# Optimization experiments

Measured on AMD Instinct MI355X. Metric: run time of the kernel, lower is better.

Reference implementation:

```python
import jax, jax.numpy as jnp
import numpy as np

VOCAB = 30522
HIDDEN = 768
MAX_POS = 512
N_TYPES = 8
N_HEADS = 4
NHID = 128
LN_EPS = 1e-12
ALPHA = 0.01  # LeakyReLU slope
NEG = -9e15


def setup_inputs() -> dict:
    key = jax.random.key(0)
    ks = jax.random.split(key, 12)
    B, N = 8, 256
    token_ids = jax.random.randint(ks[0], (B, N), 0, VOCAB)
    type_ids = jax.random.randint(ks[1], (B, N), 0, 7)
    synset_ids = jax.random.randint(ks[2], (B, N), 0, 32)
    highway = jax.random.randint(ks[3], (B, N), 0, 2).astype(bool)
    tok_emb = jax.random.normal(ks[4], (VOCAB, HIDDEN), jnp.float32) * 0.02
    type_emb = jax.random.normal(ks[5], (N_TYPES, HIDDEN), jnp.float32) * 0.02
    pos_emb = jax.random.normal(ks[6], (MAX_POS, HIDDEN), jnp.float32) * 0.02
    ln_g = jnp.ones((HIDDEN,), jnp.float32)
    ln_b = jnp.zeros((HIDDEN,), jnp.float32)
    # GAT per-head params, xavier-ish scale
    W = jax.random.normal(ks[7], (N_HEADS, HIDDEN, NHID), jnp.float32) * (1.414 * (2.0 / (HIDDEN + NHID)) ** 0.5)
    a = jax.random.normal(ks[8], (N_HEADS, 2 * NHID), jnp.float32) * (1.414 * (2.0 / (2 * NHID + 1)) ** 0.5)
    out_W = jax.random.normal(ks[9], (VOCAB, N_HEADS * NHID), jnp.float32) * 0.02
    out_b = jnp.zeros((VOCAB,), jnp.float32)
    return {"token_ids": token_ids, "type_ids": type_ids, "synset_ids": synset_ids,
            "highway": highway, "tok_emb": tok_emb, "type_emb": type_emb,
            "pos_emb": pos_emb, "ln_g": ln_g, "ln_b": ln_b, "W": W, "a": a,
            "out_W": out_W, "out_b": out_b}


def _graph_mask(token_ids, type_ids, synset_ids, highway):
    # visibility: same synset, plus directed highway edges by type
    vis = synset_ids[:, :, None] == synset_ids[:, None, :]
    t, hw = type_ids, highway
    s1 = (t == 1) & hw
    s3 = (t == 3) & hw
    d1 = (jnp.isin(t, jnp.array([0, 2, 5]))) & hw
    d3 = (jnp.isin(t, jnp.array([6, 4, 0]))) & hw
    vis = vis | (s1[:, :, None] & d1[:, None, :]) | (s3[:, :, None] & d3[:, None, :])
    not_pad = token_ids != 0  # bert padding_idx == 0
    return vis & not_pad[:, None, :]  # (B,N,N)


def reference(token_ids, type_ids, synset_ids, highway, tok_emb, type_emb,
              pos_emb, ln_g, ln_b, W, a, out_W, out_b):
    B, N = token_ids.shape
    mask = _graph_mask(token_ids, type_ids, synset_ids, highway)
    # TaxoEmbedding (eval mode: no dropout)
    x = tok_emb[token_ids] + type_emb[type_ids] + pos_emb[:N][None]
    mu = jnp.mean(x, axis=-1, keepdims=True)
    var = jnp.mean((x - mu) ** 2, axis=-1, keepdims=True)
    x = (x - mu) * jax.lax.rsqrt(var + LN_EPS) * ln_g + ln_b
    # GAT heads. e[h,b,i,j] = leakyrelu(a1_h . Wh[b,i] + a2_h . Wh[b,j])
    Wh = jnp.einsum('bnd,hdf->hbnf', x, W)  # (H,B,N,F)
    F_ = W.shape[-1]
    a1, a2 = a[:, :F_], a[:, F_:]
    e = (jnp.einsum('hbnf,hf->hbn', Wh, a1)[:, :, :, None]
         + jnp.einsum('hbnf,hf->hbn', Wh, a2)[:, :, None, :])
    e = jnp.where(e > 0, e, ALPHA * e)
    e = jnp.where(mask[None], e, NEG)
    att = jax.nn.softmax(e, axis=2)  # torch softmax(dim=1) on (B,N,N) -> i axis
    hp = jax.nn.elu(jnp.einsum('hbij,hbjf->hbif', att, Wh))  # (H,B,N,F)
    cat = hp.transpose(1, 2, 0, 3).reshape(B, N, -1)  # head-major concat
    out = jax.nn.elu(cat @ out_W.T + out_b)
    return jax.nn.log_softmax(out, axis=-1)
```

## Files before the change

### kernel.cpp

```cpp
#include <hip/hip_runtime.h>
#include <hip/hip_bf16.h>

#define VOCAB 30522
#define VPAD 30720
#define HIDDEN 768
#define NHEADS 4
#define NHID 128
#define ROWS 2048
#define KDIM 512
#define LN_EPS 1e-12f
#define ALPHA_LR 0.01f
#define NEGV -9.0e15f
#define NT256 120

typedef __attribute__((ext_vector_type(8))) short short8;
typedef __attribute__((ext_vector_type(4))) float floatx4;
typedef __attribute__((ext_vector_type(2))) float floatx2;
typedef __attribute__((ext_vector_type(4))) unsigned short ushort4v;
typedef __attribute__((ext_vector_type(8))) unsigned short ushort8v;
typedef __attribute__((ext_vector_type(4))) unsigned int uint4v;

static __device__ __forceinline__ unsigned short f2bf(float f) {
  unsigned int u = __float_as_uint(f);
  unsigned int r = u + 0x7fffu + ((u >> 16) & 1u);
  return (unsigned short)(r >> 16);
}

static __device__ __forceinline__ void gload16(const unsigned short* g, unsigned short* l) {
  __builtin_amdgcn_global_load_lds(
      (const __attribute__((address_space(1))) void*)g,
      (__attribute__((address_space(3))) void*)l, 16, 0, 0);
}

__global__ __launch_bounds__(256) void k_prep(const float* __restrict__ out_W,
    unsigned short* __restrict__ owb,
    const float* __restrict__ W, unsigned short* __restrict__ Wt,
    const int* __restrict__ tok, const int* __restrict__ typ,
    const float* __restrict__ tok_emb, const float* __restrict__ type_emb, const float* __restrict__ pos_emb,
    const float* __restrict__ ln_g, const float* __restrict__ ln_b, unsigned short* __restrict__ xout) {
  __shared__ unsigned short T[128][136];
  __shared__ float red[8];
  int bid = blockIdx.x;
  if (bid < 2048) {
    int n4src = (VOCAB * KDIM) / 4, n4tot = (VPAD * KDIM) / 4;
    int i = bid * 256 + threadIdx.x;
    int stride = 2048 * 256;
    for (; i < n4tot; i += stride) {
      ushort4v o = {0, 0, 0, 0};
      if (i < n4src) {
        floatx4 v = reinterpret_cast<const floatx4*>(out_W)[i];
        o.x = f2bf(v.x); o.y = f2bf(v.y); o.z = f2bf(v.z); o.w = f2bf(v.w);
      }
      reinterpret_cast<ushort4v*>(owb)[i] = o;
    }
  } else if (bid < 2072) {
    int b = bid - 2048;
    int h = b & 3, dc = b >> 2;
    int tid = threadIdx.x;
    const float* Wb = W + ((long)h * HIDDEN + dc * 128) * NHID;
    #pragma unroll
    for (int q = 0; q < 16; q++) {
      int idx = q * 256 + tid;
      int d = idx >> 5, f4 = idx & 31;
      floatx4 v = *reinterpret_cast<const floatx4*>(&Wb[(long)d * NHID + f4 * 4]);
      #pragma unroll
      for (int j = 0; j < 4; j++) T[f4 * 4 + j][d] = f2bf(v[j]);
    }
    __syncthreads();
    int f = tid >> 1, rh = tid & 1;
    unsigned short* dst = Wt + (long)(h * 128 + f) * HIDDEN + dc * 128 + rh * 64;
    #pragma unroll
    for (int i = 0; i < 8; i++)
      *reinterpret_cast<ushort8v*>(&dst[i * 8]) =
          *reinterpret_cast<const ushort8v*>(&T[f][rh * 64 + i * 8]);
  } else {
    int row = bid - 2072;
    int n = row & 255;
    int t = tok[row], ty = typ[row];
    const float* te = tok_emb + (long)t * HIDDEN;
    const float* ye = type_emb + (long)ty * HIDDEN;
    const float* pe = pos_emb + (long)n * HIDDEN;
    float v[3]; float s = 0.f, ss = 0.f;
    #pragma unroll
    for (int q = 0; q < 3; q++) {
      int d = threadIdx.x + q * 256;
      float x = te[d] + ye[d] + pe[d];
      v[q] = x; s += x; ss += x * x;
    }
    for (int off = 32; off; off >>= 1) { s += __shfl_down(s, off); ss += __shfl_down(ss, off); }
    int wid = threadIdx.x >> 6;
    if ((threadIdx.x & 63) == 0) { red[wid] = s; red[4 + wid] = ss; }
    __syncthreads();
    if (threadIdx.x == 0) {
      float a = red[0] + red[1] + red[2] + red[3];
      float b2 = red[4] + red[5] + red[6] + red[7];
      float mu = a * (1.0f / 768.0f);
      float var = b2 * (1.0f / 768.0f) - mu * mu;
      red[0] = mu; red[1] = rsqrtf(var + LN_EPS);
    }
    __syncthreads();
    float mu = red[0], rstd = red[1];
    #pragma unroll
    for (int q = 0; q < 3; q++) {
      int d = threadIdx.x + q * 256;
      xout[(long)row * HIDDEN + d] = f2bf((v[q] - mu) * rstd * ln_g[d] + ln_b[d]);
    }
  }
}

__global__ __launch_bounds__(256) void k_wh(const unsigned short* __restrict__ A,
    const unsigned short* __restrict__ Bw, float* __restrict__ Wh) {
  int mt = blockIdx.x & 15, nt = blockIdx.x >> 4;
  int m0 = mt * 128, n0 = nt * 128;
  __shared__ __align__(16) unsigned short Al[2][128 * 64];
  __shared__ __align__(16) unsigned short Bl[2][128 * 64];
  int tid = threadIdx.x;
  int l = tid & 63, wid = tid >> 6;
  int wr = wid >> 1, wc = wid & 1;
  int lrow = l & 15, lgrp = l >> 4;
  floatx4 acc[4][4];
  #pragma unroll
  for (int i = 0; i < 4; i++)
    #pragma unroll
    for (int j = 0; j < 4; j++) acc[i][j] = (floatx4){0.f, 0.f, 0.f, 0.f};
  const unsigned short* Ab = A + (long)m0 * HIDDEN;
  const unsigned short* Bb = Bw + (long)n0 * HIDDEN;

  auto STAGE = [&](int t, int bufi) {
    #pragma unroll
    for (int q = 0; q < 4; q++) {
      int chunk = q * 256 + tid;
      int row = chunk >> 3, kp = chunk & 7, swz = kp ^ (row & 7);
      long off = (long)row * HIDDEN + t * 64 + swz * 8;
      gload16(Ab + off, &Al[bufi][chunk * 8]);
      gload16(Bb + off, &Bl[bufi][chunk * 8]);
    }
  };

  STAGE(0, 0);
  STAGE(1, 1);
  asm volatile("s_waitcnt vmcnt(8)" ::: "memory");
  __builtin_amdgcn_sched_barrier(0);
  __builtin_amdgcn_s_barrier();

  #pragma unroll
  for (int kt = 0; kt < 12; kt++) {
    int cur = kt & 1;
    short8 af[2][4], bf[2][4];
    #pragma unroll
    for (int kk = 0; kk < 2; kk++) {
      int sA = (kk * 4 + lgrp) ^ (lrow & 7);
      #pragma unroll
      for (int mi = 0; mi < 4; mi++)
        af[kk][mi] = *reinterpret_cast<const short8*>(&Al[cur][(wr * 64 + mi * 16 + lrow) * 64 + sA * 8]);
      #pragma unroll
      for (int ni = 0; ni < 4; ni++)
        bf[kk][ni] = *reinterpret_cast<const short8*>(&Bl[cur][(wc * 64 + ni * 16 + lrow) * 64 + sA * 8]);
    }
    asm volatile("s_waitcnt lgkmcnt(0)" ::: "memory");
    __builtin_amdgcn_sched_barrier(0);
    __builtin_amdgcn_s_barrier();
    __builtin_amdgcn_sched_barrier(0);
    if (kt < 10) STAGE(kt + 2, cur);
    #pragma unroll
    for (int kk = 0; kk < 2; kk++)
      #pragma unroll
      for (int mi = 0; mi < 4; mi++)
        #pragma unroll
        for (int ni = 0; ni < 4; ni++)
          acc[mi][ni] = __builtin_amdgcn_mfma_f32_16x16x32_bf16(af[kk][mi], bf[kk][ni], acc[mi][ni], 0, 0, 0);
    if (kt < 10) {
      asm volatile("s_waitcnt vmcnt(8)" ::: "memory");
    } else if (kt == 10) {
      asm volatile("s_waitcnt vmcnt(0)" ::: "memory");
    }
    __builtin_amdgcn_sched_barrier(0);
    if (kt < 11) __builtin_amdgcn_s_barrier();
  }

  #pragma unroll
  for (int mi = 0; mi < 4; mi++) {
    #pragma unroll
    for (int reg = 0; reg < 4; reg++) {
      int row = m0 + wr * 64 + mi * 16 + lgrp * 4 + reg;
      #pragma unroll
      for (int ni = 0; ni < 4; ni++) {
        int c = n0 + wc * 64 + ni * 16 + lrow;
        int h = c >> 7, f = c & 127;
        Wh[((long)h * ROWS + row) * NHID + f] = acc[mi][ni][reg];
      }
    }
  }
}

__device__ __forceinline__ unsigned char mk_flags(int t, int hwv, int tokv) {
  unsigned char fl = 0;
  if (hwv) {
    if (t == 1) fl |= 1;
    if (t == 3) fl |= 2;
    if (t == 0 || t == 2 || t == 5) fl |= 4;
    if (t == 6 || t == 4 || t == 0) fl |= 8;
  }
  if (tokv != 0) fl |= 16;
  return fl;
}

__global__ __launch_bounds__(256) void k_ecol(const int* __restrict__ tok, const int* __restrict__ typ,
    const int* __restrict__ syn, const int* __restrict__ hw,
    const float* __restrict__ Wh, const float* __restrict__ a,
    float* __restrict__ e1, float* __restrict__ e2,
    float* __restrict__ colmax, float* __restrict__ colrs) {
  int h = blockIdx.x >> 3, b = blockIdx.x & 7;
  __shared__ float av[256];
  __shared__ float E1[256]; __shared__ int SY[256]; __shared__ unsigned char FL[256];
  int tid = threadIdx.x;
  int g = b * 256 + tid;
  av[tid] = a[h * 256 + tid];
  FL[tid] = mk_flags(typ[g], hw[g], tok[g]);
  SY[tid] = syn[g];
  __syncthreads();
  const float* wr = Wh + ((long)h * ROWS + g) * NHID;
  float s1 = 0.f, s2 = 0.f;
  #pragma unroll 8
  for (int f = 0; f < 128; f++) { float w = wr[f]; s1 += w * av[f]; s2 += w * av[128 + f]; }
  e1[h * ROWS + g] = s1; e2[h * ROWS + g] = s2;
  E1[tid] = s1;
  __syncthreads();
  float e2j = s2;
  int syj = SY[tid]; unsigned char flj = FL[tid];
  bool npj = flj & 16, d1j = flj & 4, d3j = flj & 8;
  float m = -INFINITY;
  for (int i = 0; i < 256; i++) {
    float e = E1[i] + e2j;
    e = e > 0.f ? e : ALPHA_LR * e;
    unsigned char fli = FL[i];
    bool vis = (SY[i] == syj) || ((fli & 1) && d1j) || ((fli & 2) && d3j);
    float v = (vis && npj) ? e : NEGV;
    m = fmaxf(m, v);
  }
  float s = 0.f;
  for (int i = 0; i < 256; i++) {
    float e = E1[i] + e2j;
    e = e > 0.f ? e : ALPHA_LR * e;
    unsigned char fli = FL[i];
    bool vis = (SY[i] == syj) || ((fli & 1) && d1j) || ((fli & 2) && d3j);
    float v = (vis && npj) ? e : NEGV;
    s += __expf(v - m);
  }
  int idx = (h * 8 + b) * 256 + tid;
  colmax[idx] = m;
  colrs[idx] = 1.0f / s;
}

__global__ __launch_bounds__(256) void k_att(const int* __restrict__ tok, const int* __restrict__ typ,
    const int* __restrict__ syn, const int* __restrict__ hw,
    const float* __restrict__ e1, const float* __restrict__ e2,
    const float* __restrict__ colmax, const float* __restrict__ colrs,
    const float* __restrict__ Wh, unsigned short* __restrict__ cat) {
  int chunk = blockIdx.x & 7; int hb = blockIdx.x >> 3;
  int h = hb >> 3, b = hb & 7;
  __shared__ float E2[256], CM[256], CR[256];
  __shared__ int SY[256]; __shared__ unsigned char FL[256];
  __shared__ float WJ[64][128];
  int tid = threadIdx.x;
  {
    int g = b * 256 + tid;
    FL[tid] = mk_flags(typ[g], hw[g], tok[g]);
    E2[tid] = e2[h * ROWS + g];
    CM[tid] = colmax[hb * 256 + tid];
    CR[tid] = colrs[hb * 256 + tid];
    SY[tid] = syn[g];
  }
  __syncthreads();
  int i = chunk * 32 + (tid >> 3);
  int gi = b * 256 + i;
  float e1i = e1[h * ROWS + gi];
  unsigned char fli = FL[i];
  bool s1i = fli & 1, s3i = fli & 2;
  int syni = SY[i];
  int f0 = tid & 7;
  floatx4 acc4[4];
  #pragma unroll
  for (int k2 = 0; k2 < 4; k2++) acc4[k2] = (floatx4){0.f, 0.f, 0.f, 0.f};
  for (int j0 = 0; j0 < 256; j0 += 64) {
    #pragma unroll
    for (int q = 0; q < 8; q++) {
      int e = tid + q * 256;
      int j = e >> 5, f4 = e & 31;
      *reinterpret_cast<floatx4*>(&WJ[j][f4 * 4]) =
          *reinterpret_cast<const floatx4*>(&Wh[((long)h * ROWS + b * 256 + j0 + j) * NHID + f4 * 4]);
    }
    __syncthreads();
    for (int j = 0; j < 64; j++) {
      int jj = j0 + j;
      unsigned char flj = FL[jj];
      bool vis = (syni == SY[jj]) || (s1i && (flj & 4)) || (s3i && (flj & 8));
      bool msk = vis && (flj & 16);
      float ev = e1i + E2[jj];
      ev = ev > 0.f ? ev : ALPHA_LR * ev;
      float v = msk ? ev : NEGV;
      float w = __expf(v - CM[jj]) * CR[jj];
      #pragma unroll
      for (int k2 = 0; k2 < 4; k2++) {
        floatx4 wv = *reinterpret_cast<const floatx4*>(&WJ[j][(f0 + 8 * k2) * 4]);
        acc4[k2] += wv * w;
      }
    }
    __syncthreads();
  }
  ushort4v* cr4 = reinterpret_cast<ushort4v*>(cat + (long)gi * KDIM + h * NHID);
  #pragma unroll
  for (int k2 = 0; k2 < 4; k2++) {
    ushort4v o4;
    #pragma unroll
    for (int e = 0; e < 4; e++) {
      float v = acc4[k2][e];
      v = v > 0.f ? v : __expf(v) - 1.f;
      o4[e] = f2bf(v);
    }
    cr4[f0 + 8 * k2] = o4;
  }
}

__global__ __launch_bounds__(512, 2) void k_gemm(const unsigned short* __restrict__ A,
    const unsigned short* __restrict__ Bw, const float* __restrict__ bias,
    unsigned short* __restrict__ otmp, float* __restrict__ ps) {
  int bid = blockIdx.x;
  int lin = (bid & 7) * NT256 + (bid >> 3);
  int mt = lin & 7, nt = lin >> 3;
  int m0 = mt * 256, n0 = nt * 256;
  __shared__ __align__(16) char smem[131072];
  unsigned short (*Al)[256 * 64] = reinterpret_cast<unsigned short (*)[256 * 64]>(smem);
  unsigned short (*Bl)[256 * 64] = reinterpret_cast<unsigned short (*)[256 * 64]>(smem + 65536);
  unsigned short* Cl = reinterpret_cast<unsigned short*>(smem);
  int tid = threadIdx.x;
  int l = tid & 63, wid = tid >> 6;
  int wr = wid >> 2, wc = wid & 3;
  int lrow = l & 15, lgrp = l >> 4;
  floatx4 acc[8][4];
  #pragma unroll
  for (int i = 0; i < 8; i++)
    #pragma unroll
    for (int j = 0; j < 4; j++) acc[i][j] = (floatx4){0.f, 0.f, 0.f, 0.f};
  const unsigned short* Ab = A + (long)m0 * KDIM;
  const unsigned short* Bb = Bw + (long)n0 * KDIM;

  auto STAGE = [&](int t, int bufi) {
    #pragma unroll
    for (int q = 0; q < 4; q++) {
      int chunk = q * 512 + tid;
      int row = chunk >> 3, kp = chunk & 7, swz = kp ^ (row & 7);
      long off = (long)row * KDIM + t * 64 + swz * 8;
      gload16(Ab + off, &Al[bufi][chunk * 8]);
      gload16(Bb + off, &Bl[bufi][chunk * 8]);
    }
  };

  STAGE(0, 0);
  STAGE(1, 1);
  asm volatile("s_waitcnt vmcnt(8)" ::: "memory");
  __builtin_amdgcn_sched_barrier(0);
  __builtin_amdgcn_s_barrier();

  #pragma unroll
  for (int kt = 0; kt < 8; kt++) {
    int cur = kt & 1;
    short8 afr[8];
    short8 bfr[4];
    #pragma unroll
    for (int mi = 0; mi < 4; mi++)
      #pragma unroll
      for (int ks = 0; ks < 2; ks++)
        afr[mi * 2 + ks] = *reinterpret_cast<const short8*>(
            &Al[cur][(wr * 128 + mi * 16 + lrow) * 64 + (((ks * 4 + lgrp) ^ (lrow & 7)) * 8)]);
    #pragma unroll
    for (int ni = 0; ni < 2; ni++)
      #pragma unroll
      for (int ks = 0; ks < 2; ks++)
        bfr[ni * 2 + ks] = *reinterpret_cast<const short8*>(
            &Bl[cur][(wc * 64 + ni * 16 + lrow) * 64 + (((ks * 4 + lgrp) ^ (lrow & 7)) * 8)]);
    #pragma unroll
    for (int ks = 0; ks < 2; ks++)
      #pragma unroll
      for (int mi = 0; mi < 4; mi++)
        #pragma unroll
        for (int ni = 0; ni < 2; ni++)
          acc[mi][ni] = __builtin_amdgcn_mfma_f32_16x16x32_bf16(afr[mi * 2 + ks], bfr[ni * 2 + ks], acc[mi][ni], 0, 0, 0);
    __builtin_amdgcn_sched_barrier(0);
    #pragma unroll
    for (int ni = 0; ni < 2; ni++)
      #pragma unroll
      for (int ks = 0; ks < 2; ks++)
        bfr[ni * 2 + ks] = *reinterpret_cast<const short8*>(
            &Bl[cur][(wc * 64 + (2 + ni) * 16 + lrow) * 64 + (((ks * 4 + lgrp) ^ (lrow & 7)) * 8)]);
    #pragma unroll
    for (int ks = 0; ks < 2; ks++)
      #pragma unroll
      for (int mi = 0; mi < 4; mi++)
        #pragma unroll
        for (int ni = 0; ni < 2; ni++)
          acc[mi][2 + ni] = __builtin_amdgcn_mfma_f32_16x16x32_bf16(afr[mi * 2 + ks], bfr[ni * 2 + ks], acc[mi][2 + ni], 0, 0, 0);
    __builtin_amdgcn_sched_barrier(0);
    #pragma unroll
    for (int mi = 0; mi < 4; mi++)
      #pragma unroll
      for (int ks = 0; ks < 2; ks++)
        afr[mi * 2 + ks] = *reinterpret_cast<const short8*>(
            &Al[cur][(wr * 128 + (4 + mi) * 16 + lrow) * 64 + (((ks * 4 + lgrp) ^ (lrow & 7)) * 8)]);
    #pragma unroll
    for (int ks = 0; ks < 2; ks++)
      #pragma unroll
      for (int mi = 0; mi < 4; mi++)
        #pragma unroll
        for (int ni = 0; ni < 2; ni++)
          acc[4 + mi][2 + ni] = __builtin_amdgcn_mfma_f32_16x16x32_bf16(afr[mi * 2 + ks], bfr[ni * 2 + ks], acc[4 + mi][2 + ni], 0, 0, 0);
    __builtin_amdgcn_sched_barrier(0);
    #pragma unroll
    for (int ni = 0; ni < 2; ni++)
      #pragma unroll
      for (int ks = 0; ks < 2; ks++)
        bfr[ni * 2 + ks] = *reinterpret_cast<const short8*>(
            &Bl[cur][(wc * 64 + ni * 16 + lrow) * 64 + (((ks * 4 + lgrp) ^ (lrow & 7)) * 8)]);
    asm volatile("s_waitcnt lgkmcnt(0)" ::: "memory");
    __builtin_amdgcn_sched_barrier(0);
    __builtin_amdgcn_s_barrier();
    __builtin_amdgcn_sched_barrier(0);
    if (kt < 6) STAGE(kt + 2, cur);
    #pragma unroll
    for (int ks = 0; ks < 2; ks++)
      #pragma unroll
      for (int mi = 0; mi < 4; mi++)
        #pragma unroll
        for (int ni = 0; ni < 2; ni++)
          acc[4 + mi][ni] = __builtin_amdgcn_mfma_f32_16x16x32_bf16(afr[mi * 2 + ks], bfr[ni * 2 + ks], acc[4 + mi][ni], 0, 0, 0);
    if (kt < 6) {
      asm volatile("s_waitcnt vmcnt(8)" ::: "memory");
    } else if (kt == 6) {
      asm volatile("s_waitcnt vmcnt(0)" ::: "memory");
    }
    __builtin_amdgcn_sched_barrier(0);
    if (kt < 7) __builtin_amdgcn_s_barrier();
  }
  float bcol[4];
  #pragma unroll
  for (int ni = 0; ni < 4; ni++) {
    int c = n0 + wc * 64 + ni * 16 + lrow;
    bcol[ni] = (c < VOCAB) ? bias[c] : 0.f;
  }
  #pragma unroll
  for (int mi = 0; mi < 8; mi++)
    #pragma unroll
    for (int ni = 0; ni < 4; ni++)
      #pragma unroll
      for (int reg = 0; reg < 4; reg++) {
        int r = wr * 128 + mi * 16 + lgrp * 4 + reg;
        int c = wc * 64 + ni * 16 + lrow;
        float z = acc[mi][ni][reg] + bcol[ni];
        float o = z > 0.f ? z : __expf(z) - 1.f;
        Cl[r * 256 + c] = f2bf(o);
      }
  __syncthreads();
  #pragma unroll
  for (int it = 0; it < 16; it++) {
    int idx = it * 512 + tid;
    int r = idx >> 5, c8 = (idx & 31) * 8;
    int gc = n0 + c8;
    ushort8v v = *reinterpret_cast<const ushort8v*>(&Cl[r * 256 + c8]);
    float se = 0.f;
    #pragma unroll
    for (int e = 0; e < 8; e++)
      if (gc + e < VOCAB)
        se += __expf(__uint_as_float(((unsigned int)(unsigned short)v[e]) << 16));
    #pragma unroll
    for (int off = 1; off < 32; off <<= 1) se += __shfl_xor(se, off);
    if ((idx & 31) == 0) ps[(long)(m0 + r) * 128 + nt] = se;
    unsigned short* orow = otmp + (long)(m0 + r) * 2 * VOCAB;
    if (gc + 8 <= VOCAB) {
      *reinterpret_cast<ushort8v*>(orow + gc) = v;
    } else {
      #pragma unroll
      for (int e = 0; e < 8; e++)
        if (gc + e < VOCAB) orow[gc + e] = v[e];
    }
  }
}

__global__ __launch_bounds__(128) void k_lse(const float* __restrict__ ps, float* __restrict__ lse) {
  int row = blockIdx.x;
  int tid = threadIdx.x;
  float s = (tid < NT256) ? ps[(long)row * 128 + tid] : 0.f;
  #pragma unroll
  for (int off = 1; off < 64; off <<= 1) s += __shfl_xor(s, off);
  __shared__ float red[2];
  if ((tid & 63) == 0) red[tid >> 6] = s;
  __syncthreads();
  if (tid == 0) lse[row] = logf(red[0] + red[1]);
}

__global__ __launch_bounds__(1024) void k_sub(float* __restrict__ out, const float* __restrict__ lse) {
  int row = blockIdx.x;
  float L = lse[row];
  float* rb = out + (long)row * VOCAB;
  const uint4v* src4 = reinterpret_cast<const uint4v*>(rb);
  int tid = threadIdx.x;
  uint4v v4[4];
  #pragma unroll
  for (int k = 0; k < 4; k++) {
    int p4 = tid + k * 1024;
    if (p4 < 3816) v4[k] = src4[p4];
  }
  __syncthreads();
  floatx4* dst4 = reinterpret_cast<floatx4*>(rb);
  #pragma unroll
  for (int k = 0; k < 4; k++) {
    int p4 = tid + k * 1024;
    if (p4 < 3815) {
      uint4v u = v4[k];
      floatx4 a, b;
      a.x = __uint_as_float((u.x & 0xffffu) << 16) - L;
      a.y = __uint_as_float(u.x & 0xffff0000u) - L;
      a.z = __uint_as_float((u.y & 0xffffu) << 16) - L;
      a.w = __uint_as_float(u.y & 0xffff0000u) - L;
      b.x = __uint_as_float((u.z & 0xffffu) << 16) - L;
      b.y = __uint_as_float(u.z & 0xffff0000u) - L;
      b.z = __uint_as_float((u.w & 0xffffu) << 16) - L;
      b.w = __uint_as_float(u.w & 0xffff0000u) - L;
      dst4[2 * p4] = a;
      dst4[2 * p4 + 1] = b;
    } else if (p4 == 3815) {
      unsigned int u = v4[k].x;
      rb[30520] = __uint_as_float((u & 0xffffu) << 16) - L;
      rb[30521] = __uint_as_float(u & 0xffff0000u) - L;
    }
  }
}

extern "C" void kernel_launch(void* const* d_in, const int* in_sizes, int n_in,
                              void* d_out, int out_size, void* d_ws, size_t ws_size,
                              hipStream_t stream) {
  const int* tok = (const int*)d_in[0];
  const int* typ = (const int*)d_in[1];
  const int* syn = (const int*)d_in[2];
  const int* hw  = (const int*)d_in[3];
  const float* tok_emb  = (const float*)d_in[4];
  const float* type_emb = (const float*)d_in[5];
  const float* pos_emb  = (const float*)d_in[6];
  const float* ln_g = (const float*)d_in[7];
  const float* ln_b = (const float*)d_in[8];
  const float* W    = (const float*)d_in[9];
  const float* a    = (const float*)d_in[10];
  const float* out_W = (const float*)d_in[11];
  const float* out_b = (const float*)d_in[12];
  float* out = (float*)d_out;
  char* ws = (char*)d_ws;
  unsigned short* xb = (unsigned short*)(ws + 0);
  float* Wh  = (float*)(ws + 3145728);
  float* e1  = (float*)(ws + 7340032);
  float* e2  = (float*)(ws + 7372800);
  float* cm  = (float*)(ws + 7405568);
  float* cs  = (float*)(ws + 7438336);
  unsigned short* cat = (unsigned short*)(ws + 7471104);
  unsigned short* Wt  = (unsigned short*)(ws + 9568256);
  unsigned short* owb = (unsigned short*)(ws + 10354688);
  float* ps  = (float*)(ws + 41811968);
  float* lse = (float*)(ws + 42860544);

  k_prep<<<4120, 256, 0, stream>>>(out_W, owb, W, Wt, tok, typ,
                                   tok_emb, type_emb, pos_emb, ln_g, ln_b, xb);
  k_wh<<<64, 256, 0, stream>>>(xb, Wt, Wh);
  k_ecol<<<32, 256, 0, stream>>>(tok, typ, syn, hw, Wh, a, e1, e2, cm, cs);
  k_att<<<256, 256, 0, stream>>>(tok, typ, syn, hw, e1, e2, cm, cs, Wh, cat);
  k_gemm<<<8 * NT256, 512, 0, stream>>>(cat, owb, out_b, (unsigned short*)out, ps);
  k_lse<<<2048, 128, 0, stream>>>(ps, lse);
  k_sub<<<2048, 1024, 0, stream>>>(out, lse);
}
```

Measured before the change: 313.5 us.

## Move row exp-sum from GEMM epilogue into fused log-softmax kernel

The per-tile partial exp-sum computation and its cross-lane shuffles are removed from the GEMM epilogue, and the separate k_lse kernel is dropped. k_sub now computes the row's exp-sum itself from the bf16 values already loaded into registers, reduces it across the block, takes the log, then subtracts. This removes one kernel launch, the partial-sum buffer and work in the GEMM epilogue. In exchange k_sub does more exp arithmetic and an extra block-wide reduction with a barrier.

After: 304.4 us. 2.9% less time.

```diff
diff --git a/kernel.cpp b/kernel.cpp
--- a/kernel.cpp
+++ b/kernel.cpp
@@ -324,7 +324,7 @@
 
 __global__ __launch_bounds__(512, 2) void k_gemm(const unsigned short* __restrict__ A,
     const unsigned short* __restrict__ Bw, const float* __restrict__ bias,
-    unsigned short* __restrict__ otmp, float* __restrict__ ps) {
+    unsigned short* __restrict__ otmp) {
   int bid = blockIdx.x;
   int lin = (bid & 7) * NT256 + (bid >> 3);
   int mt = lin & 7, nt = lin >> 3;
@@ -466,14 +466,6 @@
     int r = idx >> 5, c8 = (idx & 31) * 8;
     int gc = n0 + c8;
     ushort8v v = *reinterpret_cast<const ushort8v*>(&Cl[r * 256 + c8]);
-    float se = 0.f;
-    #pragma unroll
-    for (int e = 0; e < 8; e++)
-      if (gc + e < VOCAB)
-        se += __expf(__uint_as_float(((unsigned int)(unsigned short)v[e]) << 16));
-    #pragma unroll
-    for (int off = 1; off < 32; off <<= 1) se += __shfl_xor(se, off);
-    if ((idx & 31) == 0) ps[(long)(m0 + r) * 128 + nt] = se;
     unsigned short* orow = otmp + (long)(m0 + r) * 2 * VOCAB;
     if (gc + 8 <= VOCAB) {
       *reinterpret_cast<ushort8v*>(orow + gc) = v;
@@ -485,31 +477,49 @@
   }
 }
 
-__global__ __launch_bounds__(128) void k_lse(const float* __restrict__ ps, float* __restrict__ lse) {
+__global__ __launch_bounds__(1024) void k_sub(float* __restrict__ out) {
   int row = blockIdx.x;
-  int tid = threadIdx.x;
-  float s = (tid < NT256) ? ps[(long)row * 128 + tid] : 0.f;
-  #pragma unroll
-  for (int off = 1; off < 64; off <<= 1) s += __shfl_xor(s, off);
-  __shared__ float red[2];
-  if ((tid & 63) == 0) red[tid >> 6] = s;
-  __syncthreads();
-  if (tid == 0) lse[row] = logf(red[0] + red[1]);
-}
-
-__global__ __launch_bounds__(1024) void k_sub(float* __restrict__ out, const float* __restrict__ lse) {
-  int row = blockIdx.x;
-  float L = lse[row];
   float* rb = out + (long)row * VOCAB;
   const uint4v* src4 = reinterpret_cast<const uint4v*>(rb);
   int tid = threadIdx.x;
   uint4v v4[4];
+  float se = 0.f;
   #pragma unroll
   for (int k = 0; k < 4; k++) {
     int p4 = tid + k * 1024;
     if (p4 < 3816) v4[k] = src4[p4];
   }
+  #pragma unroll
+  for (int k = 0; k < 4; k++) {
+    int p4 = tid + k * 1024;
+    if (p4 < 3815) {
+      uint4v u = v4[k];
+      #pragma unroll
+      for (int e = 0; e < 4; e++) {
+        unsigned int w = u[e];
+        se += __expf(__uint_as_float((w & 0xffffu) << 16));
+        se += __expf(__uint_as_float(w & 0xffff0000u));
+      }
+    } else if (p4 == 3815) {
+      unsigned int w = v4[k].x;
+      se += __expf(__uint_as_float((w & 0xffffu) << 16));
+      se += __expf(__uint_as_float(w & 0xffff0000u));
+    }
+  }
+  #pragma unroll
+  for (int off = 32; off; off >>= 1) se += __shfl_xor(se, off);
+  __shared__ float red[16];
+  int wid = tid >> 6;
+  if ((tid & 63) == 0) red[wid] = se;
   __syncthreads();
+  if (tid < 16) {
+    float r = red[tid];
+    #pragma unroll
+    for (int off = 8; off; off >>= 1) r += __shfl_xor(r, off);
+    if (tid == 0) red[0] = logf(r);
+  }
+  __syncthreads();
+  float L = red[0];
   floatx4* dst4 = reinterpret_cast<floatx4*>(rb);
   #pragma unroll
   for (int k = 0; k < 4; k++) {
@@ -562,15 +572,12 @@
   unsigned short* cat = (unsigned short*)(ws + 7471104);
   unsigned short* Wt  = (unsigned short*)(ws + 9568256);
   unsigned short* owb = (unsigned short*)(ws + 10354688);
-  float* ps  = (float*)(ws + 41811968);
-  float* lse = (float*)(ws + 42860544);
 
   k_prep<<<4120, 256, 0, stream>>>(out_W, owb, W, Wt, tok, typ,
                                    tok_emb, type_emb, pos_emb, ln_g, ln_b, xb);
   k_wh<<<64, 256, 0, stream>>>(xb, Wt, Wh);
   k_ecol<<<32, 256, 0, stream>>>(tok, typ, syn, hw, Wh, a, e1, e2, cm, cs);
   k_att<<<256, 256, 0, stream>>>(tok, typ, syn, hw, e1, e2, cm, cs, Wh, cat);
-  k_gemm<<<8 * NT256, 512, 0, stream>>>(cat, owb, out_b, (unsigned short*)out, ps);
-  k_lse<<<2048, 128, 0, stream>>>(ps, lse);
-  k_sub<<<2048, 1024, 0, stream>>>(out, lse);
-}
+  k_gemm<<<8 * NT256, 512, 0, stream>>>(cat, owb, out_b, (unsigned short*)out);
+  k_sub<<<2048, 1024, 0, stream>>>(out);
+}
```
